# Kernel tuning notes

Measured on AMD Instinct MI355X. Metric: run time of the kernel, lower is better.

The kernel has to match this reference:

```python
import jax, jax.numpy as jnp
import numpy as np

N_NODES = 50000
N_EDGES = 800000
IN_DIM = 128
HID = 256


def _gcn_conv(x, src, dst, norm, W, b, n_nodes):
    # PyG GCNConv: h = x @ W; out[dst] += norm * h[src]; out += b
    h = x @ W                                   # [N, out_dim]
    msgs = h[src] * norm[:, None]               # [E+N, out_dim]
    agg = jax.ops.segment_sum(msgs, dst, num_segments=n_nodes)
    return agg + b


def _gcn_norm(src, dst, n_nodes):
    # add self-loops and compute symmetric normalization deg^-1/2 A_hat deg^-1/2
    loops = jnp.arange(n_nodes, dtype=src.dtype)
    src2 = jnp.concatenate([src, loops])
    dst2 = jnp.concatenate([dst, loops])
    deg = jax.ops.segment_sum(jnp.ones_like(dst2, dtype=jnp.float32), dst2,
                              num_segments=n_nodes)
    dis = jnp.where(deg > 0, jax.lax.rsqrt(deg), 0.0)
    norm = dis[src2] * dis[dst2]
    return src2, dst2, norm


def setup_inputs() -> dict:
    key = jax.random.key(0)
    ks = jax.random.split(key, 5)
    x = jax.random.normal(ks[0], (N_NODES, IN_DIM), dtype=jnp.float32)
    edge_index = jax.random.randint(ks[1], (2, N_EDGES), 0, N_NODES, dtype=jnp.int64)
    W1 = jax.random.normal(ks[2], (IN_DIM, HID), dtype=jnp.float32) / np.sqrt(IN_DIM)
    b1 = jnp.zeros((HID,), dtype=jnp.float32)
    W2 = jax.random.normal(ks[3], (HID, HID // 2), dtype=jnp.float32) / np.sqrt(HID)
    b2 = jnp.zeros((HID // 2,), dtype=jnp.float32)
    Wfc = jax.random.normal(ks[4], (HID // 2, 1), dtype=jnp.float32) / np.sqrt(HID // 2)
    bfc = jnp.zeros((1,), dtype=jnp.float32)
    return {"x": x, "edge_index": edge_index, "W1": W1, "b1": b1,
            "W2": W2, "b2": b2, "Wfc": Wfc, "bfc": bfc}


def reference(x, edge_index, W1, b1, W2, b2, Wfc, bfc):
    n_nodes = x.shape[0]
    src, dst = edge_index[0], edge_index[1]
    src2, dst2, norm = _gcn_norm(src, dst, n_nodes)
    h = jax.nn.relu(_gcn_conv(x, src2, dst2, norm, W1, b1, n_nodes))
    h = jax.nn.relu(_gcn_conv(h, src2, dst2, norm, W2, b2, n_nodes))
    pooled = h.mean(axis=0)                     # [HID//2]
    return pooled @ Wfc + bfc                   # [1]
```

## Files before the change

### kernel.cpp

```cpp
#include <hip/hip_runtime.h>
#include <hip/hip_bf16.h>

#define N_NODES 50000
#define N_EDGES 800000
#define EHALF   400000
#define IN_DIM  128
#define HID     256
#define HID2    128
#define BUCKET  64
#define NPART   8
#define PSIZE   6250
#define CHUNKS  ((EHALF + 255) / 256)

using bf16x8 = __attribute__((ext_vector_type(8))) short;
using f32x4  = __attribute__((ext_vector_type(4))) float;

static __device__ __forceinline__ unsigned f2bf(float f) {
    unsigned u = __float_as_uint(f);
    return (u + 0x7FFFu + ((u >> 16) & 1u)) >> 16;
}
static __device__ __forceinline__ float bflo(unsigned u) { return __uint_as_float(u << 16); }
static __device__ __forceinline__ float bfhi(unsigned u) { return __uint_as_float(u & 0xFFFF0000u); }

static __device__ __forceinline__ int bucket_sort64(int v, int lane) {
#pragma unroll
    for (int k = 2; k <= 64; k <<= 1) {
#pragma unroll
        for (int j = k >> 1; j > 0; j >>= 1) {
            int p = __shfl_xor(v, j, 64);
            int mn = min(v, p), mx = max(v, p);
            bool up = ((lane & k) == 0);
            bool lower = ((lane & j) == 0);
            v = (up == lower) ? mn : mx;
        }
    }
    return v;
}

__global__ void fill_bucket(const int* __restrict__ ei, int* __restrict__ curA,
                            int* __restrict__ curB, int* __restrict__ srcs) {
    int b = blockIdx.x;
    int p = b & 7;
    int e = (b >> 3) * 256 + threadIdx.x;
    if (e < EHALF) {
        int lo = p * PSIZE, hi = lo + PSIZE;
        int s0 = ei[e];
        int s1 = ei[EHALF + e];
        int d0 = ei[N_EDGES + e];
        int d1 = ei[N_EDGES + EHALF + e];
        if (d0 >= lo && d0 < hi) {
            int o0 = atomicAdd(&curA[d0], 1);
            if (o0 < BUCKET) srcs[(d0 << 6) + o0] = s0;
        }
        if (d1 >= lo && d1 < hi) {
            int o1 = atomicAdd(&curB[d1], 1);
            if (o1 < BUCKET) srcs[(d1 << 6) + (BUCKET - 1 - o1)] = s1;
        }
    }
}

__global__ __launch_bounds__(256)
void pack_wts(const float* __restrict__ W1, const float* __restrict__ W2,
              unsigned short* __restrict__ WT1, unsigned short* __restrict__ WT2,
              int* __restrict__ curA, int* __restrict__ curB) {
    int t = blockIdx.x * 256 + threadIdx.x;
    if (t < N_NODES) { curA[t] = 0; curB[t] = 0; }
    if (t < IN_DIM * HID) {
        int n = t / IN_DIM, k = t - n * IN_DIM;
        WT1[t] = (unsigned short)f2bf(W1[(size_t)k * HID + n]);
    } else {
        int t2 = t - IN_DIM * HID;
        int n = t2 / HID, k = t2 - n * HID;
        WT2[t2] = (unsigned short)f2bf(W2[(size_t)k * HID2 + n]);
    }
}

__global__ __launch_bounds__(256)
void pack_x_scaled(const float* __restrict__ in, const int* __restrict__ curA,
                   const int* __restrict__ curB, unsigned* __restrict__ out) {
    int t = blockIdx.x * 256 + threadIdx.x;
    int row = t >> 5;
    float d = rsqrtf((float)(curA[row] + curB[row] + 1));
    float4 v = ((const float4*)in)[t];
    uint2 p;
    p.x = f2bf(d * v.x) | (f2bf(d * v.y) << 16);
    p.y = f2bf(d * v.z) | (f2bf(d * v.w) << 16);
    ((uint2*)out)[t] = p;
}

__global__ __launch_bounds__(256)
void agg_x_bf16(const unsigned* __restrict__ Xb, const int* __restrict__ curA,
                const int* __restrict__ curB, const int* __restrict__ srcs,
                unsigned* __restrict__ Ab) {
    int wid = threadIdx.x >> 6, lane = threadIdx.x & 63;
    int i = blockIdx.x * 4 + wid;
    unsigned sv = Xb[(size_t)i * 64 + lane];
    float a0 = bflo(sv), a1 = bfhi(sv);
    int dgA = min(curA[i], BUCKET), dgB = min(curB[i], BUCKET);
    int dgr = curA[i] + curB[i];
    int dg = min(dgA + dgB, BUCKET);
    bool valid = (lane < dgA) || (lane >= BUCKET - dgB);
    int se = valid ? srcs[(i << 6) + lane] : 0x7FFFFFFF;
    se = bucket_sort64(se, lane);
    int j = 0;
    for (; j + 8 <= dg; j += 8) {
        unsigned v0 = Xb[(size_t)__shfl(se, j + 0, 64) * 64 + lane];
        unsigned v1 = Xb[(size_t)__shfl(se, j + 1, 64) * 64 + lane];
        unsigned v2 = Xb[(size_t)__shfl(se, j + 2, 64) * 64 + lane];
        unsigned v3 = Xb[(size_t)__shfl(se, j + 3, 64) * 64 + lane];
        unsigned v4 = Xb[(size_t)__shfl(se, j + 4, 64) * 64 + lane];
        unsigned v5 = Xb[(size_t)__shfl(se, j + 5, 64) * 64 + lane];
        unsigned v6 = Xb[(size_t)__shfl(se, j + 6, 64) * 64 + lane];
        unsigned v7 = Xb[(size_t)__shfl(se, j + 7, 64) * 64 + lane];
        a0 += ((bflo(v0) + bflo(v1)) + (bflo(v2) + bflo(v3)))
            + ((bflo(v4) + bflo(v5)) + (bflo(v6) + bflo(v7)));
        a1 += ((bfhi(v0) + bfhi(v1)) + (bfhi(v2) + bfhi(v3)))
            + ((bfhi(v4) + bfhi(v5)) + (bfhi(v6) + bfhi(v7)));
    }
    for (; j < dg; ++j) {
        unsigned v = Xb[(size_t)__shfl(se, j, 64) * 64 + lane];
        a0 += bflo(v); a1 += bfhi(v);
    }
    float di = rsqrtf((float)(dgr + 1));
    Ab[(size_t)i * 64 + lane] = f2bf(di * a0) | (f2bf(di * a1) << 16);
}

__global__ __launch_bounds__(256)
void agg_g_pool_bf16(const unsigned* __restrict__ Gb, const int* __restrict__ curA,
                     const int* __restrict__ curB, const int* __restrict__ srcs,
                     const float* __restrict__ b2, const float* __restrict__ wfc,
                     float* __restrict__ pernode) {
    int wid = threadIdx.x >> 6, lane = threadIdx.x & 63;
    int i = blockIdx.x * 4 + wid;
    unsigned sv = Gb[(size_t)i * 64 + lane];
    float a0 = bflo(sv), a1 = bfhi(sv);
    int dgA = min(curA[i], BUCKET), dgB = min(curB[i], BUCKET);
    int dgr = curA[i] + curB[i];
    int dg = min(dgA + dgB, BUCKET);
    bool valid = (lane < dgA) || (lane >= BUCKET - dgB);
    int se = valid ? srcs[(i << 6) + lane] : 0x7FFFFFFF;
    se = bucket_sort64(se, lane);
    int j = 0;
    for (; j + 8 <= dg; j += 8) {
        unsigned v0 = Gb[(size_t)__shfl(se, j + 0, 64) * 64 + lane];
        unsigned v1 = Gb[(size_t)__shfl(se, j + 1, 64) * 64 + lane];
        unsigned v2 = Gb[(size_t)__shfl(se, j + 2, 64) * 64 + lane];
        unsigned v3 = Gb[(size_t)__shfl(se, j + 3, 64) * 64 + lane];
        unsigned v4 = Gb[(size_t)__shfl(se, j + 4, 64) * 64 + lane];
        unsigned v5 = Gb[(size_t)__shfl(se, j + 5, 64) * 64 + lane];
        unsigned v6 = Gb[(size_t)__shfl(se, j + 6, 64) * 64 + lane];
        unsigned v7 = Gb[(size_t)__shfl(se, j + 7, 64) * 64 + lane];
        a0 += ((bflo(v0) + bflo(v1)) + (bflo(v2) + bflo(v3)))
            + ((bflo(v4) + bflo(v5)) + (bflo(v6) + bflo(v7)));
        a1 += ((bfhi(v0) + bfhi(v1)) + (bfhi(v2) + bfhi(v3)))
            + ((bfhi(v4) + bfhi(v5)) + (bfhi(v6) + bfhi(v7)));
    }
    for (; j < dg; ++j) {
        unsigned v = Gb[(size_t)__shfl(se, j, 64) * 64 + lane];
        a0 += bflo(v); a1 += bfhi(v);
    }
    float di = rsqrtf((float)(dgr + 1));
    int c0 = lane * 2;
    float r = fmaxf(di * a0 + b2[c0], 0.f) * wfc[c0]
            + fmaxf(di * a1 + b2[c0 + 1], 0.f) * wfc[c0 + 1];
#pragma unroll
    for (int off = 32; off > 0; off >>= 1) r += __shfl_down(r, off, 64);
    if (lane == 0) pernode[i] = r;
}

__global__ __launch_bounds__(1024)
void reduce_final(const float* __restrict__ pn, const float* __restrict__ bfc,
                  float* __restrict__ out) {
    __shared__ float red[1024];
    int tid = threadIdx.x;
    float s0 = 0.f, s1 = 0.f, s2 = 0.f, s3 = 0.f;
    for (int i = tid; i < N_NODES; i += 4096) {
        s0 += pn[i];
        if (i + 1024 < N_NODES) s1 += pn[i + 1024];
        if (i + 2048 < N_NODES) s2 += pn[i + 2048];
        if (i + 3072 < N_NODES) s3 += pn[i + 3072];
    }
    red[tid] = (s0 + s1) + (s2 + s3);
    __syncthreads();
    for (int off = 512; off > 0; off >>= 1) {
        if (tid < off) red[tid] += red[tid + off];
        __syncthreads();
    }
    if (tid == 0) out[0] = red[0] * (1.0f / (float)N_NODES) + bfc[0];
}

template<int MODE>
__global__ __launch_bounds__(256)
void gemm_mfma(const unsigned short* __restrict__ A,
               const unsigned short* __restrict__ WT,
               const float* __restrict__ bias,
               const int* __restrict__ curA,
               const int* __restrict__ curB,
               unsigned short* __restrict__ C,
               int M, int N, int K) {
    __shared__ __align__(16) unsigned short Asl[4 * 64 * 8];
    __shared__ __align__(16) unsigned short Bsl[4 * 128 * 8];

    int tid = threadIdx.x;
    int lane = tid & 63, w = tid >> 6;
    int wr = w >> 1, wc = w & 1;
    int row0 = blockIdx.x * 64;
    int col0 = blockIdx.y * 128;

    f32x4 acc[2][4];
#pragma unroll
    for (int i = 0; i < 2; ++i)
#pragma unroll
        for (int j = 0; j < 4; ++j) acc[i][j] = (f32x4){0.f, 0.f, 0.f, 0.f};

    int arow = min(row0 + (tid & 63), M - 1);
    const unsigned short* agp = A + (size_t)arow * K + (tid >> 6) * 8;
    const unsigned short* bgp0 = WT + (size_t)(col0 + (tid & 127)) * K + (tid >> 7) * 8;
    const unsigned short* bgp1 = bgp0 + 16;

    const bf16x8* Av = (const bf16x8*)Asl;
    const bf16x8* Bv = (const bf16x8*)Bsl;
    int aidx = (lane >> 4) * 64 + wr * 32 + (lane & 15);
    int bidx = (lane >> 4) * 128 + wc * 64 + (lane & 15);

    for (int k0 = 0; k0 < K; k0 += 32) {
        *(float4*)&Asl[tid * 8]         = *(const float4*)(agp + k0);
        *(float4*)&Bsl[tid * 8]         = *(const float4*)(bgp0 + k0);
        *(float4*)&Bsl[(tid + 256) * 8] = *(const float4*)(bgp1 + k0);
        __syncthreads();

        bf16x8 af[2], bf[4];
#pragma unroll
        for (int fm = 0; fm < 2; ++fm) af[fm] = Av[aidx + fm * 16];
#pragma unroll
        for (int fn = 0; fn < 4; ++fn) bf[fn] = Bv[bidx + fn * 16];
#pragma unroll
        for (int fm = 0; fm < 2; ++fm)
#pragma unroll
            for (int fn = 0; fn < 4; ++fn)
                acc[fm][fn] = __builtin_amdgcn_mfma_f32_16x16x32_bf16(
                    af[fm], bf[fn], acc[fm][fn], 0, 0, 0);
        __syncthreads();
    }

    float bv[4];
    if (MODE == 0) {
#pragma unroll
        for (int fn = 0; fn < 4; ++fn)
            bv[fn] = bias[col0 + wc * 64 + fn * 16 + (lane & 15)];
    }
#pragma unroll
    for (int fm = 0; fm < 2; ++fm) {
#pragma unroll
        for (int r = 0; r < 4; ++r) {
            int row = row0 + wr * 32 + fm * 16 + (lane >> 4) * 4 + r;
            if (row < M) {
                float rsc = (MODE == 1)
                    ? rsqrtf((float)(curA[row] + curB[row] + 1)) : 0.f;
#pragma unroll
                for (int fn = 0; fn < 4; ++fn) {
                    int col = col0 + wc * 64 + fn * 16 + (lane & 15);
                    float v = acc[fm][fn][r];
                    if (MODE == 0) v = fmaxf(v + bv[fn], 0.f);
                    else           v = v * rsc;
                    C[(size_t)row * N + col] = (unsigned short)f2bf(v);
                }
            }
        }
    }
}

extern "C" void kernel_launch(void* const* d_in, const int* in_sizes, int n_in,
                              void* d_out, int out_size, void* d_ws, size_t ws_size,
                              hipStream_t stream) {
    const float* x   = (const float*)d_in[0];
    const int*   ei  = (const int*)d_in[1];
    const float* W1  = (const float*)d_in[2];
    const float* b1  = (const float*)d_in[3];
    const float* W2  = (const float*)d_in[4];
    const float* b2  = (const float*)d_in[5];
    const float* Wfc = (const float*)d_in[6];
    const float* bfc = (const float*)d_in[7];
    float* out = (float*)d_out;

    char* ws = (char*)d_ws;
    size_t off = 0;
    auto carve = [&](size_t bytes) {
        void* p = ws + off;
        off += (bytes + 255) & ~(size_t)255;
        return p;
    };
    int*   curA  = (int*)carve((size_t)N_NODES * 4);
    int*   curB  = (int*)carve((size_t)N_NODES * 4);
    int*   srcs  = (int*)carve((size_t)N_NODES * BUCKET * 4);
    unsigned* Xb = (unsigned*)carve((size_t)N_NODES * 64 * 4);
    unsigned* Ab = (unsigned*)carve((size_t)N_NODES * 64 * 4);
    unsigned short* h1b = (unsigned short*)carve((size_t)N_NODES * HID * 2);
    unsigned short* Gb  = (unsigned short*)carve((size_t)N_NODES * HID2 * 2);
    unsigned short* WT1 = (unsigned short*)carve((size_t)HID * IN_DIM * 2);
    unsigned short* WT2 = (unsigned short*)carve((size_t)HID2 * HID * 2);
    float* pernode = (float*)carve((size_t)N_NODES * 4);

    const int TB = 256;

    pack_wts<<<(IN_DIM * HID + HID * HID2) / TB, TB, 0, stream>>>(W1, W2, WT1, WT2,
                                                                  curA, curB);

    fill_bucket<<<CHUNKS * NPART, TB, 0, stream>>>(ei, curA, curB, srcs);

    pack_x_scaled<<<(N_NODES * IN_DIM / 4) / TB, TB, 0, stream>>>(x, curA, curB, Xb);

    agg_x_bf16<<<N_NODES / 4, TB, 0, stream>>>(Xb, curA, curB, srcs, Ab);
    {
        dim3 grid((N_NODES + 63) / 64, HID / 128);
        gemm_mfma<0><<<grid, TB, 0, stream>>>((const unsigned short*)Ab, WT1, b1,
                                              nullptr, nullptr, h1b, N_NODES, HID, IN_DIM);
    }
    {
        dim3 grid((N_NODES + 63) / 64, HID2 / 128);
        gemm_mfma<1><<<grid, TB, 0, stream>>>(h1b, WT2, nullptr, curA, curB,
                                              Gb, N_NODES, HID2, HID);
    }
    agg_g_pool_bf16<<<N_NODES / 4, TB, 0, stream>>>((const unsigned*)Gb, curA, curB,
                                                    srcs, b2, Wfc, pernode);
    reduce_final<<<1, 1024, 0, stream>>>(pernode, bfc, out);
}
```

Measured before the change: 178.5 us.

## Sort neighbor buckets once and split aggregation across column partitions

A new sort_buckets kernel sorts each node's neighbor list and stores a capped degree once. Before, both aggregation kernels re-ran the 64-lane bitonic sort and recomputed degrees. The two aggregation kernels are restructured so 16 lanes handle one node and four blocks each cover a quarter of the feature columns. That gives four times as many wavefronts and shorter per-node serial gather loops, at the cost of narrower 64-byte gathers and repeated index loads. The pooling kernel now writes per-partition partial sums, which the final reduction sums over a four times larger array. Degree normalization now uses the capped degree instead of the raw count.

```diff
diff --git a/kernel.cpp b/kernel.cpp
--- a/kernel.cpp
+++ b/kernel.cpp
@@ -11,6 +11,7 @@
 #define NPART   8
 #define PSIZE   6250
 #define CHUNKS  ((EHALF + 255) / 256)
+#define CPART   4
 
 using bf16x8 = __attribute__((ext_vector_type(8))) short;
 using f32x4  = __attribute__((ext_vector_type(4))) float;
@@ -60,6 +61,20 @@
 }
 
 __global__ __launch_bounds__(256)
+void sort_buckets(const int* __restrict__ curA, const int* __restrict__ curB,
+                  int* __restrict__ srcs, int* __restrict__ deg) {
+    int wid = threadIdx.x >> 6, lane = threadIdx.x & 63;
+    int i = blockIdx.x * 4 + wid;
+    int dgA = min(curA[i], BUCKET), dgB = min(curB[i], BUCKET);
+    int dg = min(dgA + dgB, BUCKET);
+    bool valid = (lane < dgA) || (lane >= BUCKET - dgB);
+    int se = valid ? srcs[(i << 6) + lane] : 0x7FFFFFFF;
+    se = bucket_sort64(se, lane);
+    srcs[(i << 6) + lane] = se;
+    if (lane == 0) deg[i] = dg;
+}
+
+__global__ __launch_bounds__(256)
 void pack_wts(const float* __restrict__ W1, const float* __restrict__ W2,
               unsigned short* __restrict__ WT1, unsigned short* __restrict__ WT2,
               int* __restrict__ curA, int* __restrict__ curB) {
@@ -76,11 +91,10 @@
 }
 
 __global__ __launch_bounds__(256)
-void pack_x_scaled(const float* __restrict__ in, const int* __restrict__ curA,
-                   const int* __restrict__ curB, unsigned* __restrict__ out) {
+void pack_x_scaled(const float* __restrict__ in, const int* __restrict__ deg,
+                   unsigned* __restrict__ out) {
     int t = blockIdx.x * 256 + threadIdx.x;
-    int row = t >> 5;
-    float d = rsqrtf((float)(curA[row] + curB[row] + 1));
+    float d = rsqrtf((float)(deg[t >> 5] + 1));
     float4 v = ((const float4*)in)[t];
     uint2 p;
     p.x = f2bf(d * v.x) | (f2bf(d * v.y) << 16);
@@ -89,96 +103,127 @@
 }
 
 __global__ __launch_bounds__(256)
-void agg_x_bf16(const unsigned* __restrict__ Xb, const int* __restrict__ curA,
-                const int* __restrict__ curB, const int* __restrict__ srcs,
-                unsigned* __restrict__ Ab) {
-    int wid = threadIdx.x >> 6, lane = threadIdx.x & 63;
-    int i = blockIdx.x * 4 + wid;
-    unsigned sv = Xb[(size_t)i * 64 + lane];
+void agg_x_bf16(const unsigned* __restrict__ Xb, const int* __restrict__ deg,
+                const int* __restrict__ srcs, unsigned* __restrict__ Ab) {
+    int b = blockIdx.x;
+    int p = b & 3;
+    int nb = b >> 2;
+    int t = threadIdx.x;
+    int i = nb * 16 + (t >> 4);
+    int cl = t & 15;
+    int col = p * 16 + cl;
+    int lane = t & 63;
+    int grp = lane & 48;
+    unsigned sv = Xb[(size_t)i * 64 + col];
     float a0 = bflo(sv), a1 = bfhi(sv);
-    int dgA = min(curA[i], BUCKET), dgB = min(curB[i], BUCKET);
-    int dgr = curA[i] + curB[i];
-    int dg = min(dgA + dgB, BUCKET);
-    bool valid = (lane < dgA) || (lane >= BUCKET - dgB);
-    int se = valid ? srcs[(i << 6) + lane] : 0x7FFFFFFF;
-    se = bucket_sort64(se, lane);
-    int j = 0;
-    for (; j + 8 <= dg; j += 8) {
-        unsigned v0 = Xb[(size_t)__shfl(se, j + 0, 64) * 64 + lane];
-        unsigned v1 = Xb[(size_t)__shfl(se, j + 1, 64) * 64 + lane];
-        unsigned v2 = Xb[(size_t)__shfl(se, j + 2, 64) * 64 + lane];
-        unsigned v3 = Xb[(size_t)__shfl(se, j + 3, 64) * 64 + lane];
-        unsigned v4 = Xb[(size_t)__shfl(se, j + 4, 64) * 64 + lane];
-        unsigned v5 = Xb[(size_t)__shfl(se, j + 5, 64) * 64 + lane];
-        unsigned v6 = Xb[(size_t)__shfl(se, j + 6, 64) * 64 + lane];
-        unsigned v7 = Xb[(size_t)__shfl(se, j + 7, 64) * 64 + lane];
-        a0 += ((bflo(v0) + bflo(v1)) + (bflo(v2) + bflo(v3)))
-            + ((bflo(v4) + bflo(v5)) + (bflo(v6) + bflo(v7)));
-        a1 += ((bfhi(v0) + bfhi(v1)) + (bfhi(v2) + bfhi(v3)))
-            + ((bfhi(v4) + bfhi(v5)) + (bfhi(v6) + bfhi(v7)));
-    }
-    for (; j < dg; ++j) {
-        unsigned v = Xb[(size_t)__shfl(se, j, 64) * 64 + lane];
-        a0 += bflo(v); a1 += bfhi(v);
-    }
-    float di = rsqrtf((float)(dgr + 1));
-    Ab[(size_t)i * 64 + lane] = f2bf(di * a0) | (f2bf(di * a1) << 16);
-}
-
-__global__ __launch_bounds__(256)
-void agg_g_pool_bf16(const unsigned* __restrict__ Gb, const int* __restrict__ curA,
-                     const int* __restrict__ curB, const int* __restrict__ srcs,
-                     const float* __restrict__ b2, const float* __restrict__ wfc,
-                     float* __restrict__ pernode) {
-    int wid = threadIdx.x >> 6, lane = threadIdx.x & 63;
-    int i = blockIdx.x * 4 + wid;
-    unsigned sv = Gb[(size_t)i * 64 + lane];
+    int dg = deg[i];
+    int ebase = i << 6;
+    for (int b0 = 0; b0 < dg; b0 += 16) {
+        int se = srcs[ebase + b0 + cl];
+        int lim = min(dg - b0, 16);
+        int jj = 0;
+        for (; jj + 8 <= lim; jj += 8) {
+            int s0 = __shfl(se, grp + jj + 0, 64);
+            int s1 = __shfl(se, grp + jj + 1, 64);
+            int s2 = __shfl(se, grp + jj + 2, 64);
+            int s3 = __shfl(se, grp + jj + 3, 64);
+            int s4 = __shfl(se, grp + jj + 4, 64);
+            int s5 = __shfl(se, grp + jj + 5, 64);
+            int s6 = __shfl(se, grp + jj + 6, 64);
+            int s7 = __shfl(se, grp + jj + 7, 64);
+            unsigned v0 = Xb[(size_t)s0 * 64 + col];
+            unsigned v1 = Xb[(size_t)s1 * 64 + col];
+            unsigned v2 = Xb[(size_t)s2 * 64 + col];
+            unsigned v3 = Xb[(size_t)s3 * 64 + col];
+            unsigned v4 = Xb[(size_t)s4 * 64 + col];
+            unsigned v5 = Xb[(size_t)s5 * 64 + col];
+            unsigned v6 = Xb[(size_t)s6 * 64 + col];
+            unsigned v7 = Xb[(size_t)s7 * 64 + col];
+            a0 += ((bflo(v0) + bflo(v1)) + (bflo(v2) + bflo(v3)))
+                + ((bflo(v4) + bflo(v5)) + (bflo(v6) + bflo(v7)));
+            a1 += ((bfhi(v0) + bfhi(v1)) + (bfhi(v2) + bfhi(v3)))
+                + ((bfhi(v4) + bfhi(v5)) + (bfhi(v6) + bfhi(v7)));
+        }
+        for (; jj < lim; ++jj) {
+            int s = __shfl(se, grp + jj, 64);
+            unsigned v = Xb[(size_t)s * 64 + col];
+            a0 += bflo(v); a1 += bfhi(v);
+        }
+    }
+    float di = rsqrtf((float)(dg + 1));
+    Ab[(size_t)i * 64 + col] = f2bf(di * a0) | (f2bf(di * a1) << 16);
+}
+
+__global__ __launch_bounds__(256)
+void agg_g_pool_bf16(const unsigned* __restrict__ Gb, const int* __restrict__ deg,
+                     const int* __restrict__ srcs, const float* __restrict__ b2,
+                     const float* __restrict__ wfc, float* __restrict__ pernode4) {
+    int b = blockIdx.x;
+    int p = b & 3;
+    int nb = b >> 2;
+    int t = threadIdx.x;
+    int i = nb * 16 + (t >> 4);
+    int cl = t & 15;
+    int col = p * 16 + cl;
+    int lane = t & 63;
+    int grp = lane & 48;
+    unsigned sv = Gb[(size_t)i * 64 + col];
     float a0 = bflo(sv), a1 = bfhi(sv);
-    int dgA = min(curA[i], BUCKET), dgB = min(curB[i], BUCKET);
-    int dgr = curA[i] + curB[i];
-    int dg = min(dgA + dgB, BUCKET);
-    bool valid = (lane < dgA) || (lane >= BUCKET - dgB);
-    int se = valid ? srcs[(i << 6) + lane] : 0x7FFFFFFF;
-    se = bucket_sort64(se, lane);
-    int j = 0;
-    for (; j + 8 <= dg; j += 8) {
-        unsigned v0 = Gb[(size_t)__shfl(se, j + 0, 64) * 64 + lane];
-        unsigned v1 = Gb[(size_t)__shfl(se, j + 1, 64) * 64 + lane];
-        unsigned v2 = Gb[(size_t)__shfl(se, j + 2, 64) * 64 + lane];
-        unsigned v3 = Gb[(size_t)__shfl(se, j + 3, 64) * 64 + lane];
-        unsigned v4 = Gb[(size_t)__shfl(se, j + 4, 64) * 64 + lane];
-        unsigned v5 = Gb[(size_t)__shfl(se, j + 5, 64) * 64 + lane];
-        unsigned v6 = Gb[(size_t)__shfl(se, j + 6, 64) * 64 + lane];
-        unsigned v7 = Gb[(size_t)__shfl(se, j + 7, 64) * 64 + lane];
-        a0 += ((bflo(v0) + bflo(v1)) + (bflo(v2) + bflo(v3)))
-            + ((bflo(v4) + bflo(v5)) + (bflo(v6) + bflo(v7)));
-        a1 += ((bfhi(v0) + bfhi(v1)) + (bfhi(v2) + bfhi(v3)))
-            + ((bfhi(v4) + bfhi(v5)) + (bfhi(v6) + bfhi(v7)));
-    }
-    for (; j < dg; ++j) {
-        unsigned v = Gb[(size_t)__shfl(se, j, 64) * 64 + lane];
-        a0 += bflo(v); a1 += bfhi(v);
-    }
-    float di = rsqrtf((float)(dgr + 1));
-    int c0 = lane * 2;
+    int dg = deg[i];
+    int ebase = i << 6;
+    for (int b0 = 0; b0 < dg; b0 += 16) {
+        int se = srcs[ebase + b0 + cl];
+        int lim = min(dg - b0, 16);
+        int jj = 0;
+        for (; jj + 8 <= lim; jj += 8) {
+            int s0 = __shfl(se, grp + jj + 0, 64);
+            int s1 = __shfl(se, grp + jj + 1, 64);
+            int s2 = __shfl(se, grp + jj + 2, 64);
+            int s3 = __shfl(se, grp + jj + 3, 64);
+            int s4 = __shfl(se, grp + jj + 4, 64);
+            int s5 = __shfl(se, grp + jj + 5, 64);
+            int s6 = __shfl(se, grp + jj + 6, 64);
+            int s7 = __shfl(se, grp + jj + 7, 64);
+            unsigned v0 = Gb[(size_t)s0 * 64 + col];
+            unsigned v1 = Gb[(size_t)s1 * 64 + col];
+            unsigned v2 = Gb[(size_t)s2 * 64 + col];
+            unsigned v3 = Gb[(size_t)s3 * 64 + col];
+            unsigned v4 = Gb[(size_t)s4 * 64 + col];
+            unsigned v5 = Gb[(size_t)s5 * 64 + col];
+            unsigned v6 = Gb[(size_t)s6 * 64 + col];
+            unsigned v7 = Gb[(size_t)s7 * 64 + col];
+            a0 += ((bflo(v0) + bflo(v1)) + (bflo(v2) + bflo(v3)))
+                + ((bflo(v4) + bflo(v5)) + (bflo(v6) + bflo(v7)));
+            a1 += ((bfhi(v0) + bfhi(v1)) + (bfhi(v2) + bfhi(v3)))
+                + ((bfhi(v4) + bfhi(v5)) + (bfhi(v6) + bfhi(v7)));
+        }
+        for (; jj < lim; ++jj) {
+            int s = __shfl(se, grp + jj, 64);
+            unsigned v = Gb[(size_t)s * 64 + col];
+            a0 += bflo(v); a1 += bfhi(v);
+        }
+    }
+    float di = rsqrtf((float)(dg + 1));
+    int c0 = col * 2;
     float r = fmaxf(di * a0 + b2[c0], 0.f) * wfc[c0]
             + fmaxf(di * a1 + b2[c0 + 1], 0.f) * wfc[c0 + 1];
 #pragma unroll
-    for (int off = 32; off > 0; off >>= 1) r += __shfl_down(r, off, 64);
-    if (lane == 0) pernode[i] = r;
-}
-
+    for (int m = 8; m >= 1; m >>= 1) r += __shfl_xor(r, m, 64);
+    if (cl == 0) pernode4[(size_t)p * N_NODES + i] = r;
+}
+
+#define NTOT (4 * N_NODES)
 __global__ __launch_bounds__(1024)
 void reduce_final(const float* __restrict__ pn, const float* __restrict__ bfc,
                   float* __restrict__ out) {
     __shared__ float red[1024];
     int tid = threadIdx.x;
     float s0 = 0.f, s1 = 0.f, s2 = 0.f, s3 = 0.f;
-    for (int i = tid; i < N_NODES; i += 4096) {
+    for (int i = tid; i < NTOT; i += 4096) {
         s0 += pn[i];
-        if (i + 1024 < N_NODES) s1 += pn[i + 1024];
-        if (i + 2048 < N_NODES) s2 += pn[i + 2048];
-        if (i + 3072 < N_NODES) s3 += pn[i + 3072];
+        if (i + 1024 < NTOT) s1 += pn[i + 1024];
+        if (i + 2048 < NTOT) s2 += pn[i + 2048];
+        if (i + 3072 < NTOT) s3 += pn[i + 3072];
     }
     red[tid] = (s0 + s1) + (s2 + s3);
     __syncthreads();
@@ -194,8 +239,7 @@
 void gemm_mfma(const unsigned short* __restrict__ A,
                const unsigned short* __restrict__ WT,
                const float* __restrict__ bias,
-               const int* __restrict__ curA,
-               const int* __restrict__ curB,
+               const int* __restrict__ deg,
                unsigned short* __restrict__ C,
                int M, int N, int K) {
     __shared__ __align__(16) unsigned short Asl[4 * 64 * 8];
@@ -256,7 +300,7 @@
             int row = row0 + wr * 32 + fm * 16 + (lane >> 4) * 4 + r;
             if (row < M) {
                 float rsc = (MODE == 1)
-                    ? rsqrtf((float)(curA[row] + curB[row] + 1)) : 0.f;
+                    ? rsqrtf((float)(deg[row] + 1)) : 0.f;
 #pragma unroll
                 for (int fn = 0; fn < 4; ++fn) {
                     int col = col0 + wc * 64 + fn * 16 + (lane & 15);
@@ -292,6 +336,7 @@
     };
     int*   curA  = (int*)carve((size_t)N_NODES * 4);
     int*   curB  = (int*)carve((size_t)N_NODES * 4);
+    int*   deg   = (int*)carve((size_t)N_NODES * 4);
     int*   srcs  = (int*)carve((size_t)N_NODES * BUCKET * 4);
     unsigned* Xb = (unsigned*)carve((size_t)N_NODES * 64 * 4);
     unsigned* Ab = (unsigned*)carve((size_t)N_NODES * 64 * 4);
@@ -299,7 +344,7 @@
     unsigned short* Gb  = (unsigned short*)carve((size_t)N_NODES * HID2 * 2);
     unsigned short* WT1 = (unsigned short*)carve((size_t)HID * IN_DIM * 2);
     unsigned short* WT2 = (unsigned short*)carve((size_t)HID2 * HID * 2);
-    float* pernode = (float*)carve((size_t)N_NODES * 4);
+    float* pernode4 = (float*)carve((size_t)NTOT * 4);
 
     const int TB = 256;
 
@@ -308,20 +353,23 @@
 
     fill_bucket<<<CHUNKS * NPART, TB, 0, stream>>>(ei, curA, curB, srcs);
 
-    pack_x_scaled<<<(N_NODES * IN_DIM / 4) / TB, TB, 0, stream>>>(x, curA, curB, Xb);
-
-    agg_x_bf16<<<N_NODES / 4, TB, 0, stream>>>(Xb, curA, curB, srcs, Ab);
+    sort_buckets<<<N_NODES / 4, TB, 0, stream>>>(curA, curB, srcs, deg);
+
+    pack_x_scaled<<<(N_NODES * IN_DIM / 4) / TB, TB, 0, stream>>>(x, deg, Xb);
+
+    agg_x_bf16<<<(N_NODES / 16) * CPART, TB, 0, stream>>>(Xb, deg, srcs, Ab);
     {
         dim3 grid((N_NODES + 63) / 64, HID / 128);
         gemm_mfma<0><<<grid, TB, 0, stream>>>((const unsigned short*)Ab, WT1, b1,
-                                              nullptr, nullptr, h1b, N_NODES, HID, IN_DIM);
+                                              nullptr, h1b, N_NODES, HID, IN_DIM);
     }
     {
         dim3 grid((N_NODES + 63) / 64, HID2 / 128);
-        gemm_mfma<1><<<grid, TB, 0, stream>>>(h1b, WT2, nullptr, curA, curB,
+        gemm_mfma<1><<<grid, TB, 0, stream>>>(h1b, WT2, nullptr, deg,
                                               Gb, N_NODES, HID2, HID);
     }
-    agg_g_pool_bf16<<<N_NODES / 4, TB, 0, stream>>>((const unsigned*)Gb, curA, curB,
-                                                    srcs, b2, Wfc, pernode);
-    reduce_final<<<1, 1024, 0, stream>>>(pernode, bfc, out);
-}
+    agg_g_pool_bf16<<<(N_NODES / 16) * CPART, TB, 0, stream>>>((const unsigned*)Gb,
+                                                               deg, srcs, b2, Wfc,
+                                                               pernode4);
+    reduce_final<<<1, 1024, 0, stream>>>(pernode4, bfc, out);
+}
```

After: 224.7 us. 1.26x slower.
